# Kernel tuning notes

Hardware: AMD Instinct MI355X
Metric: run time of the kernel (lower is better)

## Reference

```python
import jax, jax.numpy as jnp
import numpy as np

D, M, B, K = 512, 512, 8, 16
EPS = 1e-8
LAMBDA = 1.0
BALANCE_COEFF = 0.0


def _l2_normalize(x, axis=-1):
    n = jnp.linalg.norm(x, axis=axis, keepdims=True)
    return x / jnp.maximum(n, EPS)


def setup_inputs() -> dict:
    key = jax.random.key(0)
    k1, k2, k3 = jax.random.split(key, 3)
    x = jax.random.normal(k1, (2, 2048, D), dtype=jnp.float32)
    V = jax.random.normal(k2, (D, M, B), dtype=jnp.float32)
    U = jax.random.normal(k3, (M, D + 1, B), dtype=jnp.float32)
    return {"x": x, "V": V, "U": U}


def reference(x, V, U):
    input_shape = x.shape
    x_flat = x.reshape(-1, D)                      # (N, D)
    x_flat = _l2_normalize(x_flat)
    N = x_flat.shape[0]

    # UnitColNorm: unit-norm columns of V over the D axis (dim=0)
    Vn = V / jnp.maximum(jnp.linalg.norm(V, axis=0, keepdims=True), EPS)
    # UnitColNormPadded: unit-norm columns of U over the (D+1) axis (dim=1)
    Un = U / jnp.maximum(jnp.linalg.norm(U, axis=1, keepdims=True), EPS)

    # Read: h_all (N, m, b)
    h_all = jnp.einsum('nd,dmb->nmb', x_flat, Vn)

    # Top-k expert selection by energy
    energy = jnp.sum(h_all * h_all, axis=-1)       # (N, m)
    topk_vals, topk_idxs = jax.lax.top_k(energy, K)  # (N, k)
    h_sparse = jnp.take_along_axis(h_all, topk_idxs[:, :, None], axis=1)  # (N, k, b)

    # Autoencode aux (V_active gathered under no_grad in torch)
    V_t = jnp.transpose(Vn, (1, 0, 2))             # (m, D, b)
    V_active = jax.lax.stop_gradient(V_t[topk_idxs])  # (N, k, D, b)
    x_hat = jnp.einsum('nkdb,nkb->nd', V_active, h_sparse)
    resid = x_flat - x_hat
    uncaptured_energy = jnp.mean(jnp.sum(resid * resid, axis=-1))

    avg_energy = jnp.mean(energy, axis=0)          # (m,)
    denom = jnp.maximum(jnp.sum(avg_energy), EPS)
    probs = jnp.maximum(avg_energy / denom, EPS)
    balance_entropy = -jnp.sum(probs * jnp.log(probs)) / jnp.log(jnp.float32(M))
    topk_aux_loss = uncaptured_energy + BALANCE_COEFF * (1.0 - balance_entropy)

    # expert usage counts (monitoring only)
    counts = jnp.zeros((M,), jnp.float32).at[topk_idxs.reshape(-1)].add(1.0)

    # Write: gather per-token expert U matrices, drop the padding row
    U_active = Un[topk_idxs][:, :, :D, :]          # (N, k, D, b)
    writes = jnp.einsum('nkdb,nkb->nd', U_active, h_sparse)
    h_recon = jnp.einsum('nkdb,nd->nkb', U_active, writes)
    writer_aux_loss = jnp.mean((h_recon - jax.lax.stop_gradient(h_sparse)) ** 2)

    aux_loss = topk_aux_loss + writer_aux_loss

    x_out = _l2_normalize(x_flat + LAMBDA * writes).reshape(input_shape)
    return x_out, aux_loss, counts
```

## Files before the change

kernel.cpp:

```cpp
#include <hip/hip_runtime.h>
#include <math.h>

#define N_TOK 4096
#define D_DIM 512
#define M_EXP 512
#define B_DIM 8
#define K_TOP 16
#define MB    4096
#define UROW  4104
#define EPSV  1e-8f
#define KTOT  1536

typedef unsigned short ushort8 __attribute__((ext_vector_type(8)));
typedef unsigned short ushort4v __attribute__((ext_vector_type(4)));
typedef short short8 __attribute__((ext_vector_type(8)));
typedef float f32x4 __attribute__((ext_vector_type(4)));

__device__ inline float b2f(unsigned short u) {
    union { unsigned int i; float f; } c;
    c.i = ((unsigned int)u) << 16;
    return c.f;
}
__device__ inline unsigned short f2b(float f) {
    union { float f; unsigned int i; } c; c.f = f;
    unsigned int lsb = (c.i >> 16) & 1;
    c.i += 0x7fffu + lsb;
    return (unsigned short)(c.i >> 16);
}
__device__ inline void gload_lds16(const unsigned short* g, unsigned short* l) {
    __builtin_amdgcn_global_load_lds(
        (const __attribute__((address_space(1))) unsigned int*)g,
        (__attribute__((address_space(3))) unsigned int*)l, 16, 0, 0);
}

__global__ __launch_bounds__(256) void k_norm_x_part(const float* __restrict__ x,
                                                     float* __restrict__ xn,
                                                     unsigned short* __restrict__ Abf,
                                                     int* __restrict__ counts,
                                                     const float* __restrict__ V,
                                                     const float* __restrict__ U,
                                                     float* __restrict__ partV,
                                                     float* __restrict__ partU)
{
    int blk = blockIdx.x;
    if (blk < 1024) {
        if (blk == 0) {
            counts[threadIdx.x] = 0;
            counts[threadIdx.x + 256] = 0;
        }
        int wave = threadIdx.x >> 6;
        int lane = threadIdx.x & 63;
        int n = blk * 4 + wave;
        const float4* xp = (const float4*)&x[(size_t)n * D_DIM + lane * 8];
        float4 a = xp[0], b = xp[1];
        float s = a.x*a.x + a.y*a.y + a.z*a.z + a.w*a.w
                + b.x*b.x + b.y*b.y + b.z*b.z + b.w*b.w;
        #pragma unroll
        for (int off = 1; off < 64; off <<= 1) s += __shfl_xor(s, off);
        float inv = 1.0f / fmaxf(sqrtf(s), EPSV);
        float v[8] = {a.x*inv, a.y*inv, a.z*inv, a.w*inv,
                      b.x*inv, b.y*inv, b.z*inv, b.w*inv};
        float4* op = (float4*)&xn[(size_t)n * D_DIM + lane * 8];
        op[0] = make_float4(v[0], v[1], v[2], v[3]);
        op[1] = make_float4(v[4], v[5], v[6], v[7]);
        ushort8 hi, lo;
        #pragma unroll
        for (int j = 0; j < 8; ++j) {
            unsigned short h = f2b(v[j]);
            hi[j] = h;
            lo[j] = f2b(v[j] - b2f(h));
        }
        size_t base = (size_t)n * KTOT + lane * 8;
        *(ushort8*)&Abf[base]        = hi;
        *(ushort8*)&Abf[base + 512]  = hi;
        *(ushort8*)&Abf[base + 1024] = lo;
    } else if (blk < 1280) {
        blk -= 1024;
        int s = blk >> 4;
        int t = (blk & 15) * 256 + threadIdx.x;
        float sum = 0.f;
        int d0 = s * 32;
        #pragma unroll 8
        for (int d = d0; d < d0 + 32; ++d) {
            float v = V[(size_t)d * MB + t];
            sum += v * v;
        }
        partV[(size_t)s * MB + t] = sum;
    } else {
        blk -= 1280;
        int s = blk >> 4;
        int t = (blk & 15) * 256 + threadIdx.x;
        int m = t >> 3, b = t & 7;
        size_t base = (size_t)m * UROW + b;
        int pbeg = s * 32;
        int pend = (s == 15) ? 513 : pbeg + 32;
        float sum = 0.f;
        for (int p = pbeg; p < pend; ++p) {
            float u = U[base + (size_t)p * 8];
            sum += u * u;
        }
        partU[(size_t)s * MB + t] = sum;
    }
}

__global__ __launch_bounds__(256) void k_norm_UV2(const float* __restrict__ V,
                                                  const float* __restrict__ U,
                                                  const float* __restrict__ partV,
                                                  const float* __restrict__ partU,
                                                  unsigned short* __restrict__ Btbf,
                                                  unsigned short* __restrict__ WXt,
                                                  unsigned short* __restrict__ U2t)
{
    int blk = blockIdx.x;
    if (blk < 256) {
        int s = blk >> 4;
        int t = (blk & 15) * 256 + threadIdx.x;
        float n2 = 0.f;
        #pragma unroll
        for (int i = 0; i < 16; ++i) n2 += partV[(size_t)i * MB + t];
        float inv = 1.0f / fmaxf(sqrtf(n2), EPSV);
        size_t row = (size_t)t * KTOT;
        int dbeg = s * 32;
        for (int d0 = dbeg; d0 < dbeg + 32; d0 += 8) {
            ushort8 hi, lo;
            #pragma unroll
            for (int j = 0; j < 8; ++j) {
                float f = V[(size_t)(d0 + j) * MB + t] * inv;
                unsigned short h = f2b(f);
                hi[j] = h;
                lo[j] = f2b(f - b2f(h));
                WXt[(size_t)(512 + d0 + j) * MB + t] = h;
            }
            *(ushort8*)&Btbf[row + d0]        = hi;
            *(ushort8*)&Btbf[row + 512 + d0]  = lo;
            *(ushort8*)&Btbf[row + 1024 + d0] = hi;
        }
    } else {
        blk -= 256;
        int s = blk >> 4;
        int t = (blk & 15) * 256 + threadIdx.x;
        int m = t >> 3, b = t & 7;
        size_t base = (size_t)m * UROW + b;
        float n2 = 0.f;
        #pragma unroll
        for (int i = 0; i < 16; ++i) n2 += partU[(size_t)i * MB + t];
        float inv = 1.0f / fmaxf(sqrtf(n2), EPSV);
        int pbeg = s * 32;
        for (int p0 = pbeg; p0 < pbeg + 32; p0 += 8) {
            ushort8 h8;
            #pragma unroll
            for (int j = 0; j < 8; ++j) {
                unsigned short h = f2b(U[base + (size_t)(p0 + j) * 8] * inv);
                h8[j] = h;
                WXt[(size_t)(p0 + j) * MB + t] = h;
            }
            *(ushort8*)&U2t[(size_t)t * D_DIM + p0] = h8;
        }
    }
}

template<int KROW, int BUF, int KC, int MH, bool READB, int SBUF, int SOP, int SKC, bool DOVM>
__device__ __forceinline__ void gemm_phase(const unsigned short* __restrict__ A,
                                           const unsigned short* __restrict__ Bt,
                                           unsigned short (*lds)[2][2][8192],
                                           f32x4 (&acc)[8][4], short8 (&bfr)[4],
                                           int wr, int wc, int lane, int wid,
                                           int brow, int bcol, int stile)
{
    const unsigned short* aun = lds[BUF][0][KC];
    const unsigned short* bun = lds[BUF][1][KC];
    int ko = ((lane >> 4) ^ ((lane >> 1) & 3)) * 8;
    short8 af[4];
    #pragma unroll
    for (int mi = 0; mi < 4; ++mi) {
        int rowL = wr * 128 + (MH * 4 + mi) * 16 + (lane & 15);
        af[mi] = *(const short8*)&aun[rowL * 32 + ko];
    }
    if (READB) {
        #pragma unroll
        for (int ni = 0; ni < 4; ++ni) {
            int colL = wc * 64 + ni * 16 + (lane & 15);
            bfr[ni] = *(const short8*)&bun[colL * 32 + ko];
        }
    }
    {
        const unsigned short* src = SOP ? Bt : A;
        int rbase = SOP ? bcol : brow;
        #pragma unroll
        for (int j = 0; j < 2; ++j) {
            int c = wid * 128 + j * 64 + lane;
            int row = c >> 2, k8 = c & 3;
            int k8s = k8 ^ ((row >> 1) & 3);
            const unsigned short* gp = src + (size_t)(rbase + row) * KROW
                                     + stile * 64 + SKC * 32 + k8s * 8;
            unsigned short* lp = lds[SBUF][SOP][SKC] + (wid * 128 + j * 64) * 8;
            gload_lds16(gp, lp);
        }
    }
    __builtin_amdgcn_s_barrier();
    __builtin_amdgcn_s_setprio(1);
    #pragma unroll
    for (int mi = 0; mi < 4; ++mi)
        #pragma unroll
        for (int ni = 0; ni < 4; ++ni)
            acc[MH * 4 + mi][ni] = __builtin_amdgcn_mfma_f32_16x16x32_bf16(
                af[mi], bfr[ni], acc[MH * 4 + mi][ni], 0, 0, 0);
    __builtin_amdgcn_s_setprio(0);
    if (DOVM) asm volatile("s_waitcnt vmcnt(4)" ::: "memory");
    __builtin_amdgcn_s_barrier();
    __builtin_amdgcn_sched_barrier(0);
}

template<int KROW, int KLEN, int NCOLT, int SPLITK, int LDC, int OUTMODE>
__global__ __launch_bounds__(512, 1) void k_gemm8(const unsigned short* __restrict__ A,
                                                  const unsigned short* __restrict__ Bt,
                                                  float* __restrict__ C,
                                                  unsigned short* __restrict__ Cb)
{
    __shared__ unsigned short lds[2][2][2][8192];

    constexpr int KT   = KLEN / 64;
    constexpr int NIT  = KLEN / 128;
    constexpr int ROWT = 16;
    constexpr int NWG  = ROWT * NCOLT * SPLITK;

    int tid = threadIdx.x;
    int wid = tid >> 6;
    int lane = tid & 63;
    int wr = wid >> 2, wc = wid & 3;

    int bid = blockIdx.x;
    int swz = (bid & 7) * (NWG / 8) + (bid >> 3);
    int ks   = swz / (ROWT * NCOLT);
    int tile = swz % (ROWT * NCOLT);
    int brow = (tile / NCOLT) * 256;
    int bcol = (tile % NCOLT) * 256;

    const unsigned short* Aofs = A + (size_t)ks * KLEN;
    const unsigned short* Bofs = Bt + (size_t)ks * KLEN;
    float* Cofs = C + (size_t)ks * 4096 * LDC;

    f32x4 acc[8][4] = {};
    short8 bfr[4];

    auto stage0 = [&](int sbuf, int sop, int skc, int stile) {
        const unsigned short* src = sop ? Bofs : Aofs;
        int rbase = sop ? bcol : brow;
        #pragma unroll
        for (int j = 0; j < 2; ++j) {
            int c = wid * 128 + j * 64 + lane;
            int row = c >> 2, k8 = c & 3;
            int k8s = k8 ^ ((row >> 1) & 3);
            const unsigned short* gp = src + (size_t)(rbase + row) * KROW
                                     + stile * 64 + skc * 32 + k8s * 8;
            unsigned short* lp = lds[sbuf][sop][skc] + (wid * 128 + j * 64) * 8;
            gload_lds16(gp, lp);
        }
    };
    stage0(0, 0, 0, 0); stage0(0, 1, 0, 0);
    stage0(0, 0, 1, 0); stage0(0, 1, 1, 0);
    stage0(1, 0, 0, 1); stage0(1, 1, 0, 1);
    asm volatile("s_waitcnt vmcnt(4)" ::: "memory");
    __builtin_amdgcn_s_barrier();
    __builtin_amdgcn_sched_barrier(0);

    for (int i = 0; i < NIT; ++i) {
        int t1 = 2 * i + 1; if (t1 > KT - 1) t1 = KT - 1;
        int t2 = 2 * i + 2; if (t2 > KT - 1) t2 = KT - 1;
        int t3 = 2 * i + 3; if (t3 > KT - 1) t3 = KT - 1;
        gemm_phase<KROW, 0, 0, 0, true , 1, 0, 1, false>(Aofs, Bofs, lds, acc, bfr, wr, wc, lane, wid, brow, bcol, t1);
        gemm_phase<KROW, 0, 0, 1, false, 1, 1, 1, false>(Aofs, Bofs, lds, acc, bfr, wr, wc, lane, wid, brow, bcol, t1);
        gemm_phase<KROW, 0, 1, 0, true , 0, 0, 0, false>(Aofs, Bofs, lds, acc, bfr, wr, wc, lane, wid, brow, bcol, t2);
        gemm_phase<KROW, 0, 1, 1, false, 0, 1, 0, true >(Aofs, Bofs, lds, acc, bfr, wr, wc, lane, wid, brow, bcol, t2);
        gemm_phase<KROW, 1, 0, 0, true , 0, 0, 1, false>(Aofs, Bofs, lds, acc, bfr, wr, wc, lane, wid, brow, bcol, t2);
        gemm_phase<KROW, 1, 0, 1, false, 0, 1, 1, false>(Aofs, Bofs, lds, acc, bfr, wr, wc, lane, wid, brow, bcol, t2);
        gemm_phase<KROW, 1, 1, 0, true , 1, 0, 0, false>(Aofs, Bofs, lds, acc, bfr, wr, wc, lane, wid, brow, bcol, t3);
        gemm_phase<KROW, 1, 1, 1, false, 1, 1, 0, true >(Aofs, Bofs, lds, acc, bfr, wr, wc, lane, wid, brow, bcol, t3);
    }

    if (OUTMODE == 0 || OUTMODE == 2) {
        #pragma unroll
        for (int mr = 0; mr < 8; ++mr) {
            int row0 = brow + wr * 128 + mr * 16 + (lane >> 4) * 4;
            #pragma unroll
            for (int nr = 0; nr < 4; ++nr) {
                int col = bcol + wc * 64 + nr * 16 + (lane & 15);
                #pragma unroll
                for (int r = 0; r < 4; ++r) {
                    if (OUTMODE == 0)
                        Cofs[(size_t)(row0 + r) * LDC + col] = acc[mr][nr][r];
                    else
                        Cb[(size_t)(row0 + r) * LDC + col] = f2b(acc[mr][nr][r]);
                }
            }
        }
    } else if (OUTMODE == 3) {
        #pragma unroll
        for (int mr = 0; mr < 8; ++mr) {
            int row0 = brow + wr * 128 + mr * 16 + (lane >> 4) * 4;
            #pragma unroll
            for (int nr = 0; nr < 4; ++nr) {
                int col = bcol + wc * 64 + nr * 16 + (lane & 15);
                f32x4 a = acc[mr][nr];
                #pragma unroll
                for (int r = 0; r < 4; ++r)
                    Cb[(size_t)(row0 + r) * 4096 + col] = f2b(a[r]);
                f32x4 sq;
                #pragma unroll
                for (int r = 0; r < 4; ++r) sq[r] = a[r] * a[r];
                #pragma unroll
                for (int off = 1; off <= 4; off <<= 1) {
                    sq[0] += __shfl_xor(sq[0], off);
                    sq[1] += __shfl_xor(sq[1], off);
                    sq[2] += __shfl_xor(sq[2], off);
                    sq[3] += __shfl_xor(sq[3], off);
                }
                if ((lane & 7) == 0) {
                    int e = ((bcol + wc * 64 + nr * 16) >> 3) + ((lane >> 3) & 1);
                    #pragma unroll
                    for (int r = 0; r < 4; ++r)
                        C[(size_t)(row0 + r) * 512 + e] = sq[r];
                }
            }
        }
    } else {
        float local = 0.f;
        #pragma unroll
        for (int mr = 0; mr < 8; ++mr) {
            int row0 = brow + wr * 128 + mr * 16 + (lane >> 4) * 4;
            #pragma unroll
            for (int nr = 0; nr < 4; ++nr) {
                int col = bcol + wc * 64 + nr * 16 + (lane & 15);
                #pragma unroll
                for (int r = 0; r < 4; ++r) {
                    unsigned short hbits = Cb[(size_t)(row0 + r) * 4096 + col];
                    if (hbits & 0x7fffu) {
                        float d = acc[mr][nr][r] - b2f(hbits);
                        local += d * d;
                    }
                }
            }
        }
        __syncthreads();
        float* red = (float*)lds;
        red[tid] = local;
        __syncthreads();
        for (int s = 256; s > 0; s >>= 1) {
            if (tid < s) red[tid] += red[tid + s];
            __syncthreads();
        }
        if (tid == 0) C[bid] = red[0];
    }
}

__global__ __launch_bounds__(256) void k_topk2(const float* __restrict__ energy,
                                               unsigned short* __restrict__ hbf,
                                               int* __restrict__ topk_idx,
                                               int* __restrict__ counts)
{
    int wave = threadIdx.x >> 6;
    int lane = threadIdx.x & 63;
    int n = blockIdx.x * 4 + wave;
    float ev[8];
    #pragma unroll
    for (int i = 0; i < 8; ++i) ev[i] = energy[(size_t)n * M_EXP + i * 64 + lane];
    for (int r = 0; r < K_TOP; ++r) {
        float bv = -1.0f; int bi = 0;
        #pragma unroll
        for (int i = 0; i < 8; ++i) {
            if (ev[i] > bv) { bv = ev[i]; bi = i * 64 + lane; }
        }
        #pragma unroll
        for (int off = 1; off < 64; off <<= 1) {
            float ov = __shfl_xor(bv, off);
            int   oi = __shfl_xor(bi, off);
            if (ov > bv || (ov == bv && oi < bi)) { bv = ov; bi = oi; }
        }
        if (lane == 0) {
            topk_idx[n * K_TOP + r] = bi;
            atomicAdd(&counts[bi], 1);
        }
        #pragma unroll
        for (int i = 0; i < 8; ++i)
            if (((bi >> 6) == i) && (lane == (bi & 63))) ev[i] = -INFINITY;
    }
    ushort8 z = {0, 0, 0, 0, 0, 0, 0, 0};
    #pragma unroll
    for (int i = 0; i < 8; ++i) {
        int e = i * 64 + lane;
        if (ev[i] != -INFINITY)
            *(ushort8*)&hbf[(size_t)n * MB + e * 8] = z;
    }
}

__global__ __launch_bounds__(256) void k_reduce_fin(const float* __restrict__ P,
                                                    const float* __restrict__ xn,
                                                    float* __restrict__ x_out,
                                                    unsigned short* __restrict__ wb,
                                                    float* __restrict__ uncap)
{
    const size_t S = (size_t)4096 * 1024;
    int n = blockIdx.x;
    int t = threadIdx.x;
    int c = t * 4;
    size_t base = (size_t)n * 1024 + c;
    float4 a = *(const float4*)&P[base];
    float4 b = *(const float4*)&P[base + S];
    float4 cc = *(const float4*)&P[base + 2 * S];
    float4 d = *(const float4*)&P[base + 3 * S];
    float4 v = make_float4(a.x + b.x + cc.x + d.x, a.y + b.y + cc.y + d.y,
                           a.z + b.z + cc.z + d.z, a.w + b.w + cc.w + d.w);
    bool isW = (c < 512);
    int xc = isW ? c : (c - 512);
    float4 xv = *(const float4*)&xn[(size_t)n * D_DIM + xc];
    float4 yr;
    if (isW) yr = make_float4(xv.x + v.x, xv.y + v.y, xv.z + v.z, xv.w + v.w);
    else     yr = make_float4(xv.x - v.x, xv.y - v.y, xv.z - v.z, xv.w - v.w);
    float local = yr.x*yr.x + yr.y*yr.y + yr.z*yr.z + yr.w*yr.w;

    __shared__ float red[256];
    __shared__ float sinv;
    red[t] = local;
    __syncthreads();
    for (int s = 64; s > 0; s >>= 1) {
        if ((t & 127) < s) red[t] += red[t + s];
        __syncthreads();
    }
    if (t == 0) {
        uncap[n] = red[128];
        sinv = 1.0f / fmaxf(sqrtf(red[0]), EPSV);
    }
    __syncthreads();
    if (isW) {
        float inv = sinv;
        *(float4*)&x_out[(size_t)n * D_DIM + c] =
            make_float4(yr.x*inv, yr.y*inv, yr.z*inv, yr.w*inv);
        ushort4v o;
        o[0] = f2b(yr.x); o[1] = f2b(yr.y); o[2] = f2b(yr.z); o[3] = f2b(yr.w);
        *(ushort4v*)&wb[(size_t)n * 512 + c] = o;
    }
}

__global__ __launch_bounds__(256) void k_finalize(const float* __restrict__ uncap,
                                                  const float* __restrict__ writer_part,
                                                  const int* __restrict__ counts,
                                                  float* __restrict__ out)
{
    __shared__ float ru[256], rw[256];
    int t = threadIdx.x;
    float su = 0.f;
    for (int i = t; i < N_TOK; i += 256) su += uncap[i];
    float sw = writer_part[t];
    ru[t] = su; rw[t] = sw;
    __syncthreads();
    for (int s = 128; s > 0; s >>= 1) {
        if (t < s) { ru[t] += ru[t + s]; rw[t] += rw[t + s]; }
        __syncthreads();
    }
    if (t == 0)
        out[(size_t)N_TOK * D_DIM] = ru[0] / (float)N_TOK
                                   + rw[0] / (float)(N_TOK * K_TOP * B_DIM);
    for (int i = t; i < M_EXP; i += 256)
        out[(size_t)N_TOK * D_DIM + 1 + i] = (float)counts[i];
}

extern "C" void kernel_launch(void* const* d_in, const int* in_sizes, int n_in,
                              void* d_out, int out_size, void* d_ws, size_t ws_size,
                              hipStream_t stream)
{
    const float* x = (const float*)d_in[0];
    const float* V = (const float*)d_in[1];
    const float* U = (const float*)d_in[2];
    float* out = (float*)d_out;

    float* ws     = (float*)d_ws;
    float* xn     = ws;
    float* P      = xn + 2097152;
    float* uncap  = P + 16777216;
    float* writer_part = uncap + 4096;
    int*   topk_i = (int*)(writer_part + 512);
    int*   counts = topk_i + 65536;
    float* partV  = (float*)(counts + 1024);
    float* partU  = partV + 65536;
    unsigned short* hbf = (unsigned short*)(partU + 65536);
    unsigned short* U2t = hbf + 16777216;
    unsigned short* WXt = U2t + 2097152;
    unsigned short* R   = WXt + 4194304;
    unsigned short* Abf  = R;
    unsigned short* Btbf = R + 6291456;
    unsigned short* writesb = R;
    float* energy = P;

    k_norm_x_part<<<1536, 256, 0, stream>>>(x, xn, Abf, counts, V, U, partV, partU);
    k_norm_UV2  <<<512, 256, 0, stream>>>(V, U, partV, partU, Btbf, WXt, U2t);
    k_gemm8<KTOT, KTOT, 16, 1, 4096, 3><<<256, 512, 0, stream>>>(Abf, Btbf, energy, hbf);
    k_topk2     <<<N_TOK / 4, 256, 0, stream>>>(energy, hbf, topk_i, counts);
    k_gemm8<4096, 1024, 4, 4, 1024, 0><<<256, 512, 0, stream>>>(hbf, WXt, P, nullptr);
    k_reduce_fin<<<4096, 256, 0, stream>>>(P, xn, out, writesb, uncap);
    k_gemm8<D_DIM, D_DIM, 16, 1, 4096, 4><<<256, 512, 0, stream>>>(writesb, U2t, writer_part, hbf);
    k_finalize  <<<1, 256, 0, stream>>>(uncap, writer_part, counts, out);
}
```

Before: 213.0 us.

## Store x_hat split-K partials as fp16 and retile first GEMM block mapping

The split-K GEMM that produces writes and x_hat partials now writes the x_hat half as fp16 into a separate buffer and keeps the writes half in fp32. The reduce kernel reads and sums the narrower partials, so the round trip through memory between the two kernels carries fewer bytes. The first GEMM also gets a new block-to-tile mapping, which groups tiles for better L2 locality. The fp16 partials lose precision in the uncaptured-energy residual.

```diff
diff --git a/kernel.cpp b/kernel.cpp
--- a/kernel.cpp
+++ b/kernel.cpp
@@ -26,6 +26,16 @@
     unsigned int lsb = (c.i >> 16) & 1;
     c.i += 0x7fffu + lsb;
     return (unsigned short)(c.i >> 16);
+}
+__device__ inline unsigned short f2h(float f) {
+    union { _Float16 h; unsigned short u; } c;
+    c.h = (_Float16)f;
+    return c.u;
+}
+__device__ inline float h2f(unsigned short u) {
+    union { _Float16 h; unsigned short u; } c;
+    c.u = u;
+    return (float)c.h;
 }
 __device__ inline void gload_lds16(const unsigned short* g, unsigned short* l) {
     __builtin_amdgcn_global_load_lds(
@@ -230,15 +240,24 @@
     int wr = wid >> 2, wc = wid & 3;
 
     int bid = blockIdx.x;
-    int swz = (bid & 7) * (NWG / 8) + (bid >> 3);
-    int ks   = swz / (ROWT * NCOLT);
-    int tile = swz % (ROWT * NCOLT);
-    int brow = (tile / NCOLT) * 256;
-    int bcol = (tile % NCOLT) * 256;
+    int brow, bcol, ks;
+    if constexpr (NCOLT == 16 && SPLITK == 1) {
+        int x = bid & 7, p = bid >> 3;
+        brow = ((x & 3) * 4 + (p >> 3)) * 256;
+        bcol = ((x >> 2) * 8 + (p & 7)) * 256;
+        ks = 0;
+    } else {
+        int swz = (bid & 7) * (NWG / 8) + (bid >> 3);
+        ks   = swz / (ROWT * NCOLT);
+        int tile = swz % (ROWT * NCOLT);
+        brow = (tile / NCOLT) * 256;
+        bcol = (tile % NCOLT) * 256;
+    }
 
     const unsigned short* Aofs = A + (size_t)ks * KLEN;
     const unsigned short* Bofs = Bt + (size_t)ks * KLEN;
     float* Cofs = C + (size_t)ks * 4096 * LDC;
+    unsigned short* Xofs = (OUTMODE == 5) ? (Cb + (size_t)ks * 4096 * 512) : Cb;
 
     f32x4 acc[8][4] = {};
     short8 bfr[4];
@@ -291,6 +310,23 @@
                         Cofs[(size_t)(row0 + r) * LDC + col] = acc[mr][nr][r];
                     else
                         Cb[(size_t)(row0 + r) * LDC + col] = f2b(acc[mr][nr][r]);
+                }
+            }
+        }
+    } else if (OUTMODE == 5) {
+        #pragma unroll
+        for (int mr = 0; mr < 8; ++mr) {
+            int row0 = brow + wr * 128 + mr * 16 + (lane >> 4) * 4;
+            #pragma unroll
+            for (int nr = 0; nr < 4; ++nr) {
+                int col = bcol + wc * 64 + nr * 16 + (lane & 15);
+                #pragma unroll
+                for (int r = 0; r < 4; ++r) {
+                    float v = acc[mr][nr][r];
+                    if (col < 512)
+                        Cofs[(size_t)(row0 + r) * 512 + col] = v;
+                    else
+                        Xofs[(size_t)(row0 + r) * 512 + (col - 512)] = f2h(v);
                 }
             }
         }
@@ -393,25 +429,39 @@
     }
 }
 
-__global__ __launch_bounds__(256) void k_reduce_fin(const float* __restrict__ P,
+__global__ __launch_bounds__(256) void k_reduce_fin(const float* __restrict__ Wp,
+                                                    const unsigned short* __restrict__ Xp,
                                                     const float* __restrict__ xn,
                                                     float* __restrict__ x_out,
                                                     unsigned short* __restrict__ wb,
                                                     float* __restrict__ uncap)
 {
-    const size_t S = (size_t)4096 * 1024;
+    const size_t S = (size_t)4096 * 512;
     int n = blockIdx.x;
     int t = threadIdx.x;
     int c = t * 4;
-    size_t base = (size_t)n * 1024 + c;
-    float4 a = *(const float4*)&P[base];
-    float4 b = *(const float4*)&P[base + S];
-    float4 cc = *(const float4*)&P[base + 2 * S];
-    float4 d = *(const float4*)&P[base + 3 * S];
-    float4 v = make_float4(a.x + b.x + cc.x + d.x, a.y + b.y + cc.y + d.y,
-                           a.z + b.z + cc.z + d.z, a.w + b.w + cc.w + d.w);
     bool isW = (c < 512);
     int xc = isW ? c : (c - 512);
+    float4 v;
+    if (isW) {
+        size_t base = (size_t)n * 512 + c;
+        float4 a = *(const float4*)&Wp[base];
+        float4 b = *(const float4*)&Wp[base + S];
+        float4 cc = *(const float4*)&Wp[base + 2 * S];
+        float4 d = *(const float4*)&Wp[base + 3 * S];
+        v = make_float4(a.x + b.x + cc.x + d.x, a.y + b.y + cc.y + d.y,
+                        a.z + b.z + cc.z + d.z, a.w + b.w + cc.w + d.w);
+    } else {
+        size_t base = (size_t)n * 512 + xc;
+        ushort4v a = *(const ushort4v*)&Xp[base];
+        ushort4v b = *(const ushort4v*)&Xp[base + S];
+        ushort4v cc = *(const ushort4v*)&Xp[base + 2 * S];
+        ushort4v d = *(const ushort4v*)&Xp[base + 3 * S];
+        v = make_float4(h2f(a[0]) + h2f(b[0]) + h2f(cc[0]) + h2f(d[0]),
+                        h2f(a[1]) + h2f(b[1]) + h2f(cc[1]) + h2f(d[1]),
+                        h2f(a[2]) + h2f(b[2]) + h2f(cc[2]) + h2f(d[2]),
+                        h2f(a[3]) + h2f(b[3]) + h2f(cc[3]) + h2f(d[3]));
+    }
     float4 xv = *(const float4*)&xn[(size_t)n * D_DIM + xc];
     float4 yr;
     if (isW) yr = make_float4(xv.x + v.x, xv.y + v.y, xv.z + v.z, xv.w + v.w);
@@ -490,13 +540,15 @@
     unsigned short* Btbf = R + 6291456;
     unsigned short* writesb = R;
     float* energy = P;
+    float* Wp = P;
+    unsigned short* Xp = (unsigned short*)(P + 4 * 4096 * 512);
 
     k_norm_x_part<<<1536, 256, 0, stream>>>(x, xn, Abf, counts, V, U, partV, partU);
     k_norm_UV2  <<<512, 256, 0, stream>>>(V, U, partV, partU, Btbf, WXt, U2t);
     k_gemm8<KTOT, KTOT, 16, 1, 4096, 3><<<256, 512, 0, stream>>>(Abf, Btbf, energy, hbf);
     k_topk2     <<<N_TOK / 4, 256, 0, stream>>>(energy, hbf, topk_i, counts);
-    k_gemm8<4096, 1024, 4, 4, 1024, 0><<<256, 512, 0, stream>>>(hbf, WXt, P, nullptr);
-    k_reduce_fin<<<4096, 256, 0, stream>>>(P, xn, out, writesb, uncap);
+    k_gemm8<4096, 1024, 4, 4, 512, 5><<<256, 512, 0, stream>>>(hbf, WXt, Wp, Xp);
+    k_reduce_fin<<<4096, 256, 0, stream>>>(Wp, Xp, xn, out, writesb, uncap);
     k_gemm8<D_DIM, D_DIM, 16, 1, 4096, 4><<<256, 512, 0, stream>>>(writesb, U2t, writer_part, hbf);
     k_finalize  <<<1, 256, 0, stream>>>(uncap, writer_part, counts, out);
 }
```

New measurement: 210.7 us. About the same (-1.1%).
